# Kernel tuning notes

Hardware: AMD Instinct MI355X
Metric: run time of the kernel (lower is better)

## Reference

```python
import jax, jax.numpy as jnp
import numpy as np

B, N, D = 8, 4096, 1024
S, K = 4, 16            # n_slices, per-slice codebook size (2^(16/4))
d = D // S              # slice_dim = 256
BETA = 0.25


def setup_inputs() -> dict:
    key = jax.random.key(0)
    k1, k2 = jax.random.split(key)
    h = jax.random.normal(k1, (B, N, D), dtype=jnp.float32)
    # nn.init.uniform_(codebook.weight, -1/K, 1/K)
    codebooks = jax.random.uniform(k2, (S, K, d), dtype=jnp.float32,
                                   minval=-1.0 / K, maxval=1.0 / K)
    return {"h": h, "codebooks": codebooks}


def reference(h, codebooks):
    Bb, Nn, Dd = h.shape
    Ss, Kk, dd = codebooks.shape
    sg = jax.lax.stop_gradient

    # sliced DVQ: view h as [B,N,S,d]
    ze = h.reshape(Bb, Nn, Ss, dd)

    # pairwise squared distances per slice: [B,N,S,K]
    dist = ((ze ** 2).sum(-1, keepdims=True)
            + (codebooks ** 2).sum(-1)[None, None, :, :]
            - 2.0 * jnp.einsum('bnsd,skd->bnsk', ze, codebooks))
    ids = jnp.argmin(dist, axis=-1)                         # [B,N,S] int

    # gather nearest codes: [B,N,S,d]
    zq = codebooks[jnp.arange(Ss)[None, None, :], ids]

    # per-slice VQ losses (mse over that slice), summed over slices
    loss_cb = jnp.mean((zq - sg(ze)) ** 2, axis=(0, 1, 3))  # [S]
    loss_cm = jnp.mean((ze - sg(zq)) ** 2, axis=(0, 1, 3))  # [S]
    vq_total = (loss_cb + BETA * loss_cm).sum()

    # straight-through estimator, concat slices back to [B,N,D]
    z = (ze + sg(zq - ze)).reshape(Bb, Nn, Dd)

    # pack ids: offsets are [1, K, K^2, K^3] since all slice sizes equal
    offsets = (Kk ** jnp.arange(Ss)).astype(jnp.int32)
    ids_packed = (ids.astype(jnp.int32) * offsets).sum(-1)  # [B,N]

    return (z, ids_packed, vq_total)
```

## Files before the change

### kernel.cpp

```cpp
#include <hip/hip_runtime.h>


#define D_FULL 1024
#define SEG 4
#define DSEG 256
#define KC 16

__global__ __launch_bounds__(256) void dvq_prep(const float* __restrict__ cb,
                                                double* __restrict__ cbd,
                                                double* __restrict__ c2d,
                                                float* __restrict__ ids_out,
                                                float* __restrict__ loss_out) {
    __shared__ double ws[4];
    const int b = blockIdx.x;
    const int t = threadIdx.x;
    const int lane = t & 63;
    const int w = t >> 6;

    cbd[b * 256 + t] = (double)cb[b * 256 + t];

    ids_out[b * 512 + t] = 0.0f;
    ids_out[b * 512 + 256 + t] = 0.0f;
    if (b == 0 && t == 0) *loss_out = 0.0f;

    double v = (double)cb[b * 256 + t];
    double sq = v * v;
#pragma unroll
    for (int off = 32; off > 0; off >>= 1)
        sq += __shfl_down(sq, off, 64);
    if (lane == 0) ws[w] = sq;
    __syncthreads();
    if (t == 0) c2d[b] = ws[0] + ws[1] + ws[2] + ws[3];
}

__global__ __launch_bounds__(256) void dvq_main(const float* __restrict__ h,
                                                const float* __restrict__ cb,
                                                const double* __restrict__ cbd,
                                                const double* __restrict__ c2d,
                                                float* __restrict__ z_out,
                                                float* __restrict__ ids_out,
                                                float* __restrict__ loss_out) {
    __shared__ __align__(16) double cbl[KC * DSEG];
    __shared__ int ids_lds[64];

    const int i = threadIdx.x;
    const int lane = i & 63;
    const int w = i >> 6;
    const int ch = __builtin_amdgcn_readfirstlane(w);

    const int s = blockIdx.x & 3;
    const long tok_base = (long)(blockIdx.x >> 2) * 64;
    const long tok = tok_base + lane;

    {
        const double* src = cbd + s * (KC * DSEG);
#pragma unroll
        for (int jj = 0; jj < 16; ++jj)
            cbl[jj * 256 + i] = src[jj * 256 + i];
    }
    __syncthreads();

    const float4* zp = (const float4*)(h + tok * D_FULL + (long)s * DSEG + ch * 64);
    const double* cbs = cbl + ch * 64;

    double dot[KC];
#pragma unroll
    for (int k = 0; k < KC; ++k) dot[k] = 0.0;
    double ze2 = 0.0;

#pragma unroll 4
    for (int j = 0; j < 16; ++j) {
        float4 z4 = zp[j];
        double z0 = (double)z4.x, z1 = (double)z4.y;
        double z2 = (double)z4.z, z3 = (double)z4.w;
        ze2 = fma(z0, z0, ze2);
        ze2 = fma(z1, z1, ze2);
        ze2 = fma(z2, z2, ze2);
        ze2 = fma(z3, z3, ze2);
#pragma unroll
        for (int k = 0; k < KC; ++k) {
            const double* ck = cbs + k * DSEG + j * 4;
            double a = dot[k];
            a = fma(z0, ck[0], a);
            a = fma(z1, ck[1], a);
            a = fma(z2, ck[2], a);
            a = fma(z3, ck[3], a);
            dot[k] = a;
        }
    }

    __syncthreads();
    double* part = (double*)cbl;
    if (w != 0) {
        double* p = part + ((w - 1) * 64 + lane) * (KC + 1);
#pragma unroll
        for (int k = 0; k < KC; ++k) p[k] = dot[k];
        p[KC] = ze2;
    }
    __syncthreads();

    if (w == 0) {
#pragma unroll
        for (int c = 0; c < 3; ++c) {
            const double* p = part + (c * 64 + lane) * (KC + 1);
#pragma unroll
            for (int k = 0; k < KC; ++k) dot[k] += p[k];
            ze2 += p[KC];
        }

        const double* c2s = c2d + s * KC;
        double best = c2s[0] - 2.0 * dot[0];
        int bk = 0;
#pragma unroll
        for (int k = 1; k < KC; ++k) {
            double sc = c2s[k] - 2.0 * dot[k];
            if (sc < best) { best = sc; bk = k; }
        }
        ids_lds[lane] = bk;

        atomicAdd(&ids_out[tok], (float)(bk << (4 * s)));

        double mind = ze2 + best;
#pragma unroll
        for (int off = 32; off > 0; off >>= 1)
            mind += __shfl_down(mind, off, 64);
        if (lane == 0)
            atomicAdd(loss_out, (float)(mind * (1.25 / 8388608.0)));
    }
    __syncthreads();

    const float4* cbf4 = (const float4*)cb;
#pragma unroll 4
    for (int r0 = 0; r0 < 16; ++r0) {
        int r = ch * 16 + r0;
        int k = ids_lds[r];
        float4 v = cbf4[(s * KC + k) * (DSEG / 4) + lane];
        ((float4*)(z_out + (tok_base + r) * D_FULL + (long)s * DSEG))[lane] = v;
    }
}

extern "C" void kernel_launch(void* const* d_in, const int* in_sizes, int n_in,
                              void* d_out, int out_size, void* d_ws, size_t ws_size,
                              hipStream_t stream) {
    const float* h  = (const float*)d_in[0];
    const float* cb = (const float*)d_in[1];

    const int n_h = in_sizes[0];
    const int tokens = n_h / D_FULL;

    float* z_out    = (float*)d_out;
    float* ids_out  = z_out + (size_t)n_h;
    float* loss_out = ids_out + tokens;

    double* cbd = (double*)d_ws;
    double* c2d = cbd + SEG * KC * DSEG;

    dvq_prep<<<64, 256, 0, stream>>>(cb, cbd, c2d, ids_out, loss_out);
    dvq_main<<<(tokens / 64) * SEG, 256, 0, stream>>>(h, cb, cbd, c2d, z_out,
                                                      ids_out, loss_out);
}
```

Measured before the change: 261.4 us.

## Process two tokens per thread and keep codebook in LDS as float

Each block now handles 128 tokens instead of 64, so every codebook value read from LDS is reused for two tokens' dot products. The codebook is staged in LDS as fp32 and converted to double in registers, which halves the LDS footprint and removes the separate double-conversion pass in the prep kernel. The reduction is done twice through a smaller shared partial-sum arena, and loss atomics are halved. The cost is more registers for two sets of 16 double accumulators, which may limit occupancy despite the launch bound hint.

```diff
diff --git a/kernel.cpp b/kernel.cpp
--- a/kernel.cpp
+++ b/kernel.cpp
@@ -7,7 +7,6 @@
 #define KC 16
 
 __global__ __launch_bounds__(256) void dvq_prep(const float* __restrict__ cb,
-                                                double* __restrict__ cbd,
                                                 double* __restrict__ c2d,
                                                 float* __restrict__ ids_out,
                                                 float* __restrict__ loss_out) {
@@ -16,8 +15,6 @@
     const int t = threadIdx.x;
     const int lane = t & 63;
     const int w = t >> 6;
-
-    cbd[b * 256 + t] = (double)cb[b * 256 + t];
 
     ids_out[b * 512 + t] = 0.0f;
     ids_out[b * 512 + 256 + t] = 0.0f;
@@ -33,15 +30,14 @@
     if (t == 0) c2d[b] = ws[0] + ws[1] + ws[2] + ws[3];
 }
 
-__global__ __launch_bounds__(256) void dvq_main(const float* __restrict__ h,
-                                                const float* __restrict__ cb,
-                                                const double* __restrict__ cbd,
-                                                const double* __restrict__ c2d,
-                                                float* __restrict__ z_out,
-                                                float* __restrict__ ids_out,
-                                                float* __restrict__ loss_out) {
-    __shared__ __align__(16) double cbl[KC * DSEG];
-    __shared__ int ids_lds[64];
+__global__ __launch_bounds__(256, 4) void dvq_main(const float* __restrict__ h,
+                                                   const float* __restrict__ cb,
+                                                   const double* __restrict__ c2d,
+                                                   float* __restrict__ z_out,
+                                                   float* __restrict__ ids_out,
+                                                   float* __restrict__ loss_out) {
+    __shared__ __align__(16) double arena[3 * 64 * (KC + 1)];
+    __shared__ int ids_lds[128];
 
     const int i = threadIdx.x;
     const int lane = i & 63;
@@ -49,90 +45,132 @@
     const int ch = __builtin_amdgcn_readfirstlane(w);
 
     const int s = blockIdx.x & 3;
-    const long tok_base = (long)(blockIdx.x >> 2) * 64;
-    const long tok = tok_base + lane;
+    const long tok_base = (long)(blockIdx.x >> 2) * 128;
+    const long tokA = tok_base + lane;
+    const long tokB = tokA + 64;
+
+    float* cbl = reinterpret_cast<float*>(arena);
 
     {
-        const double* src = cbd + s * (KC * DSEG);
+        const float4* src = reinterpret_cast<const float4*>(cb + s * (KC * DSEG));
+        float4* dst = reinterpret_cast<float4*>(cbl);
 #pragma unroll
         for (int jj = 0; jj < 16; ++jj)
-            cbl[jj * 256 + i] = src[jj * 256 + i];
+            dst[jj * 256 + i] = src[jj * 256 + i];
     }
     __syncthreads();
 
-    const float4* zp = (const float4*)(h + tok * D_FULL + (long)s * DSEG + ch * 64);
-    const double* cbs = cbl + ch * 64;
+    const float4* zpA = (const float4*)(h + tokA * D_FULL + (long)s * DSEG + ch * 64);
+    const float4* zpB = (const float4*)(h + tokB * D_FULL + (long)s * DSEG + ch * 64);
+    const float* cbs = cbl + ch * 64;
 
-    double dot[KC];
+    double dotA[KC], dotB[KC];
 #pragma unroll
-    for (int k = 0; k < KC; ++k) dot[k] = 0.0;
-    double ze2 = 0.0;
+    for (int k = 0; k < KC; ++k) { dotA[k] = 0.0; dotB[k] = 0.0; }
+    double zeA = 0.0, zeB = 0.0;
 
 #pragma unroll 4
     for (int j = 0; j < 16; ++j) {
-        float4 z4 = zp[j];
-        double z0 = (double)z4.x, z1 = (double)z4.y;
-        double z2 = (double)z4.z, z3 = (double)z4.w;
-        ze2 = fma(z0, z0, ze2);
-        ze2 = fma(z1, z1, ze2);
-        ze2 = fma(z2, z2, ze2);
-        ze2 = fma(z3, z3, ze2);
+        float4 a4 = zpA[j];
+        float4 b4 = zpB[j];
+        double a0 = (double)a4.x, a1 = (double)a4.y;
+        double a2 = (double)a4.z, a3 = (double)a4.w;
+        double b0 = (double)b4.x, b1 = (double)b4.y;
+        double b2 = (double)b4.z, b3 = (double)b4.w;
+        zeA = fma(a0, a0, zeA); zeA = fma(a1, a1, zeA);
+        zeA = fma(a2, a2, zeA); zeA = fma(a3, a3, zeA);
+        zeB = fma(b0, b0, zeB); zeB = fma(b1, b1, zeB);
+        zeB = fma(b2, b2, zeB); zeB = fma(b3, b3, zeB);
 #pragma unroll
         for (int k = 0; k < KC; ++k) {
-            const double* ck = cbs + k * DSEG + j * 4;
-            double a = dot[k];
-            a = fma(z0, ck[0], a);
-            a = fma(z1, ck[1], a);
-            a = fma(z2, ck[2], a);
-            a = fma(z3, ck[3], a);
-            dot[k] = a;
+            float4 c4 = *(const float4*)(cbs + k * DSEG + j * 4);
+            double c0 = (double)c4.x, c1 = (double)c4.y;
+            double c2 = (double)c4.z, c3 = (double)c4.w;
+            double a = dotA[k];
+            a = fma(a0, c0, a); a = fma(a1, c1, a);
+            a = fma(a2, c2, a); a = fma(a3, c3, a);
+            dotA[k] = a;
+            double b = dotB[k];
+            b = fma(b0, c0, b); b = fma(b1, c1, b);
+            b = fma(b2, c2, b); b = fma(b3, c3, b);
+            dotB[k] = b;
         }
     }
 
     __syncthreads();
-    double* part = (double*)cbl;
+    double* part = arena;
+    const double* c2s = c2d + s * KC;
+    double loss_acc = 0.0;
+
     if (w != 0) {
         double* p = part + ((w - 1) * 64 + lane) * (KC + 1);
 #pragma unroll
-        for (int k = 0; k < KC; ++k) p[k] = dot[k];
-        p[KC] = ze2;
+        for (int k = 0; k < KC; ++k) p[k] = dotA[k];
+        p[KC] = zeA;
     }
     __syncthreads();
-
     if (w == 0) {
 #pragma unroll
         for (int c = 0; c < 3; ++c) {
             const double* p = part + (c * 64 + lane) * (KC + 1);
 #pragma unroll
-            for (int k = 0; k < KC; ++k) dot[k] += p[k];
-            ze2 += p[KC];
+            for (int k = 0; k < KC; ++k) dotA[k] += p[k];
+            zeA += p[KC];
         }
-
-        const double* c2s = c2d + s * KC;
-        double best = c2s[0] - 2.0 * dot[0];
+        double best = c2s[0] - 2.0 * dotA[0];
         int bk = 0;
 #pragma unroll
         for (int k = 1; k < KC; ++k) {
-            double sc = c2s[k] - 2.0 * dot[k];
+            double sc = c2s[k] - 2.0 * dotA[k];
             if (sc < best) { best = sc; bk = k; }
         }
         ids_lds[lane] = bk;
+        atomicAdd(&ids_out[tokA], (float)(bk << (4 * s)));
+        double mind = zeA + best;
+#pragma unroll
+        for (int off = 32; off > 0; off >>= 1)
+            mind += __shfl_down(mind, off, 64);
+        loss_acc = mind;
+    }
+    __syncthreads();
 
-        atomicAdd(&ids_out[tok], (float)(bk << (4 * s)));
-
-        double mind = ze2 + best;
+    if (w != 0) {
+        double* p = part + ((w - 1) * 64 + lane) * (KC + 1);
+#pragma unroll
+        for (int k = 0; k < KC; ++k) p[k] = dotB[k];
+        p[KC] = zeB;
+    }
+    __syncthreads();
+    if (w == 0) {
+#pragma unroll
+        for (int c = 0; c < 3; ++c) {
+            const double* p = part + (c * 64 + lane) * (KC + 1);
+#pragma unroll
+            for (int k = 0; k < KC; ++k) dotB[k] += p[k];
+            zeB += p[KC];
+        }
+        double best = c2s[0] - 2.0 * dotB[0];
+        int bk = 0;
+#pragma unroll
+        for (int k = 1; k < KC; ++k) {
+            double sc = c2s[k] - 2.0 * dotB[k];
+            if (sc < best) { best = sc; bk = k; }
+        }
+        ids_lds[64 + lane] = bk;
+        atomicAdd(&ids_out[tokB], (float)(bk << (4 * s)));
+        double mind = zeB + best;
 #pragma unroll
         for (int off = 32; off > 0; off >>= 1)
             mind += __shfl_down(mind, off, 64);
         if (lane == 0)
-            atomicAdd(loss_out, (float)(mind * (1.25 / 8388608.0)));
+            atomicAdd(loss_out, (float)((loss_acc + mind) * (1.25 / 8388608.0)));
     }
     __syncthreads();
 
     const float4* cbf4 = (const float4*)cb;
 #pragma unroll 4
-    for (int r0 = 0; r0 < 16; ++r0) {
-        int r = ch * 16 + r0;
+    for (int r0 = 0; r0 < 32; ++r0) {
+        int r = ch * 32 + r0;
         int k = ids_lds[r];
         float4 v = cbf4[(s * KC + k) * (DSEG / 4) + lane];
         ((float4*)(z_out + (tok_base + r) * D_FULL + (long)s * DSEG))[lane] = v;
@@ -152,10 +190,9 @@
     float* ids_out  = z_out + (size_t)n_h;
     float* loss_out = ids_out + tokens;
 
-    double* cbd = (double*)d_ws;
-    double* c2d = cbd + SEG * KC * DSEG;
+    double* c2d = (double*)d_ws;
 
-    dvq_prep<<<64, 256, 0, stream>>>(cb, cbd, c2d, ids_out, loss_out);
-    dvq_main<<<(tokens / 64) * SEG, 256, 0, stream>>>(h, cb, cbd, c2d, z_out,
-                                                      ids_out, loss_out);
+    dvq_prep<<<64, 256, 0, stream>>>(cb, c2d, ids_out, loss_out);
+    dvq_main<<<(tokens / 128) * SEG, 256, 0, stream>>>(h, cb, c2d, z_out,
+                                                       ids_out, loss_out);
 }
```

Measured after the change: 268.5 us. 2.7% more time.

## Stage h tile in LDS with coalesced loads, keep fp32 codebook in LDS

Applied to the files above, without the earlier changes.

The h tile for each block is now loaded with coalesced float4 reads (each wave reads whole token rows) into a swizzled LDS buffer, replacing per-thread strided float4 reads of each token's slice. The codebook is kept in LDS as fp32 and converted to double at use, which halves its LDS footprint and removes the fp64 copy made in the prep kernel. The gathered zq rows are read from LDS instead of global memory. The cost is a 64 KB LDS allocation per block, which may limit occupancy, plus extra conversion instructions in the inner loop.

```diff
diff --git a/kernel.cpp b/kernel.cpp
--- a/kernel.cpp
+++ b/kernel.cpp
@@ -7,7 +7,6 @@
 #define KC 16
 
 __global__ __launch_bounds__(256) void dvq_prep(const float* __restrict__ cb,
-                                                double* __restrict__ cbd,
                                                 double* __restrict__ c2d,
                                                 float* __restrict__ ids_out,
                                                 float* __restrict__ loss_out) {
@@ -16,8 +15,6 @@
     const int t = threadIdx.x;
     const int lane = t & 63;
     const int w = t >> 6;
-
-    cbd[b * 256 + t] = (double)cb[b * 256 + t];
 
     ids_out[b * 512 + t] = 0.0f;
     ids_out[b * 512 + 256 + t] = 0.0f;
@@ -35,13 +32,12 @@
 
 __global__ __launch_bounds__(256) void dvq_main(const float* __restrict__ h,
                                                 const float* __restrict__ cb,
-                                                const double* __restrict__ cbd,
                                                 const double* __restrict__ c2d,
                                                 float* __restrict__ z_out,
                                                 float* __restrict__ ids_out,
                                                 float* __restrict__ loss_out) {
-    __shared__ __align__(16) double cbl[KC * DSEG];
-    __shared__ int ids_lds[64];
+    __shared__ __align__(16) float4 hl[64 * 64];
+    __shared__ __align__(16) float cbl[KC * DSEG];
 
     const int i = threadIdx.x;
     const int lane = i & 63;
@@ -50,18 +46,36 @@
 
     const int s = blockIdx.x & 3;
     const long tok_base = (long)(blockIdx.x >> 2) * 64;
-    const long tok = tok_base + lane;
 
     {
-        const double* src = cbd + s * (KC * DSEG);
+        const float4* src = reinterpret_cast<const float4*>(cb + s * (KC * DSEG));
+        float4* dst = reinterpret_cast<float4*>(cbl);
 #pragma unroll
-        for (int jj = 0; jj < 16; ++jj)
-            cbl[jj * 256 + i] = src[jj * 256 + i];
+        for (int jj = 0; jj < 4; ++jj)
+            dst[jj * 256 + i] = src[jj * 256 + i];
+    }
+
+    {
+#pragma unroll
+        for (int half = 0; half < 2; ++half) {
+            float4 tmp[8];
+#pragma unroll
+            for (int rr = 0; rr < 8; ++rr) {
+                const int r = ch * 16 + half * 8 + rr;
+                tmp[rr] = *(const float4*)(h + (tok_base + r) * D_FULL +
+                                           (long)s * DSEG + lane * 4);
+            }
+#pragma unroll
+            for (int rr = 0; rr < 8; ++rr) {
+                const int r = ch * 16 + half * 8 + rr;
+                hl[r * 64 + (lane ^ r)] = tmp[rr];
+            }
+        }
     }
     __syncthreads();
 
-    const float4* zp = (const float4*)(h + tok * D_FULL + (long)s * DSEG + ch * 64);
-    const double* cbs = cbl + ch * 64;
+    const float* cbs = cbl + ch * 64;
+    const int tk = lane;
 
     double dot[KC];
 #pragma unroll
@@ -70,7 +84,8 @@
 
 #pragma unroll 4
     for (int j = 0; j < 16; ++j) {
-        float4 z4 = zp[j];
+        const int jj = ch * 16 + j;
+        float4 z4 = hl[tk * 64 + (jj ^ tk)];
         double z0 = (double)z4.x, z1 = (double)z4.y;
         double z2 = (double)z4.z, z3 = (double)z4.w;
         ze2 = fma(z0, z0, ze2);
@@ -79,18 +94,19 @@
         ze2 = fma(z3, z3, ze2);
 #pragma unroll
         for (int k = 0; k < KC; ++k) {
-            const double* ck = cbs + k * DSEG + j * 4;
+            float4 c4 = *(const float4*)(cbs + k * DSEG + j * 4);
             double a = dot[k];
-            a = fma(z0, ck[0], a);
-            a = fma(z1, ck[1], a);
-            a = fma(z2, ck[2], a);
-            a = fma(z3, ck[3], a);
+            a = fma(z0, (double)c4.x, a);
+            a = fma(z1, (double)c4.y, a);
+            a = fma(z2, (double)c4.z, a);
+            a = fma(z3, (double)c4.w, a);
             dot[k] = a;
         }
     }
 
     __syncthreads();
-    double* part = (double*)cbl;
+    double* part = (double*)hl;
+    int* ids_l = (int*)((char*)hl + 26112);
     if (w != 0) {
         double* p = part + ((w - 1) * 64 + lane) * (KC + 1);
 #pragma unroll
@@ -116,9 +132,9 @@
             double sc = c2s[k] - 2.0 * dot[k];
             if (sc < best) { best = sc; bk = k; }
         }
-        ids_lds[lane] = bk;
+        ids_l[lane] = bk;
 
-        atomicAdd(&ids_out[tok], (float)(bk << (4 * s)));
+        atomicAdd(&ids_out[tok_base + lane], (float)(bk << (4 * s)));
 
         double mind = ze2 + best;
 #pragma unroll
@@ -129,12 +145,12 @@
     }
     __syncthreads();
 
-    const float4* cbf4 = (const float4*)cb;
+    const float4* cbl4 = (const float4*)cbl;
 #pragma unroll 4
     for (int r0 = 0; r0 < 16; ++r0) {
         int r = ch * 16 + r0;
-        int k = ids_lds[r];
-        float4 v = cbf4[(s * KC + k) * (DSEG / 4) + lane];
+        int k = ids_l[r];
+        float4 v = cbl4[k * 64 + lane];
         ((float4*)(z_out + (tok_base + r) * D_FULL + (long)s * DSEG))[lane] = v;
     }
 }
@@ -152,10 +168,9 @@
     float* ids_out  = z_out + (size_t)n_h;
     float* loss_out = ids_out + tokens;
 
-    double* cbd = (double*)d_ws;
-    double* c2d = cbd + SEG * KC * DSEG;
+    double* c2d = (double*)d_ws;
 
-    dvq_prep<<<64, 256, 0, stream>>>(cb, cbd, c2d, ids_out, loss_out);
-    dvq_main<<<(tokens / 64) * SEG, 256, 0, stream>>>(h, cb, cbd, c2d, z_out,
+    dvq_prep<<<64, 256, 0, stream>>>(cb, c2d, ids_out, loss_out);
+    dvq_main<<<(tokens / 64) * SEG, 256, 0, stream>>>(h, cb, c2d, z_out,
                                                       ids_out, loss_out);
 }
```

New measurement: 270.1 us. +3.3%, slower.
